# Performance work log

Hardware: AMD Instinct MI355X
Metric: run time of the kernel (lower is better)

## Reference

```python
import jax, jax.numpy as jnp
import numpy as np

N, F = 12288, 512
NEG_INF = jnp.float32(-1e9)  # matches Keras BaseDenseAttention mask additive constant


def setup_inputs() -> dict:
    key = jax.random.key(0)
    k1, k2 = jax.random.split(key)
    features = jax.random.normal(k1, (N, F), dtype=jnp.float32)
    A = jax.random.randint(k2, (N, N), 0, 2).astype(jnp.int32)
    return {"features": features, "A": A}


def reference(features, A):
    # Keras Attention with query=key=value=dropout(features); dropout is identity
    # at inference. use_scale=False -> plain dot-product scores, no 1/sqrt(d).
    scores = jnp.einsum("nf,mf->nm", features, features)          # [N, N]
    scores = jnp.where(A > 0, scores, NEG_INF)                    # mask non-edges
    attn = jax.nn.softmax(scores, axis=-1)                        # softmax over keys
    return jnp.einsum("nm,mf->nf", attn, features)                # [N, F]
```

## Files before the change

kernel.cpp:

```cpp
#include <hip/hip_runtime.h>
#include <cstddef>
#include <cstdint>

#define NN 12288
#define FF 512
#define NWORDS (NN / 32)
#define NKT (NN / 128)

using half8 = __attribute__((ext_vector_type(8))) _Float16;
using half4 = __attribute__((ext_vector_type(4))) _Float16;
using f32x4 = __attribute__((ext_vector_type(4))) float;

constexpr float MASK_NEG = -1e9f;

__device__ __forceinline__ void gll16(const void* g, void* l) {
    __builtin_amdgcn_global_load_lds((const __attribute__((address_space(1))) void*)g,
                                     (__attribute__((address_space(3))) void*)l, 16, 0, 0);
}

#define PHASE(N)                                                        \
    do {                                                                \
        asm volatile("s_waitcnt vmcnt(" #N ")" ::: "memory");           \
        __builtin_amdgcn_s_barrier();                                   \
        __builtin_amdgcn_sched_barrier(0);                              \
    } while (0)

__global__ __launch_bounds__(256)
void compress_mask_kernel(const int* __restrict__ Amat, uint32_t* __restrict__ Abits) {
    const size_t W = (size_t)blockIdx.x * blockDim.x + threadIdx.x;
    const int4* p = reinterpret_cast<const int4*>(Amat + W * 32);
    uint32_t b = 0;
#pragma unroll
    for (int q = 0; q < 8; ++q) {
        const int4 v = p[q];
        b |= (uint32_t)(v.x > 0) << (4 * q + 0);
        b |= (uint32_t)(v.y > 0) << (4 * q + 1);
        b |= (uint32_t)(v.z > 0) << (4 * q + 2);
        b |= (uint32_t)(v.w > 0) << (4 * q + 3);
    }
    Abits[W] = b;
}

__global__ __launch_bounds__(256)
void prep_feat_kernel(const float* __restrict__ in, _Float16* __restrict__ feath,
                      _Float16* __restrict__ featT) {
    __shared__ float tile[32][33];
    const int bi = blockIdx.x;
    const int bj = blockIdx.y;
    const int r  = threadIdx.x >> 3;
    const int c4 = (threadIdx.x & 7) << 2;
    float4 v = *reinterpret_cast<const float4*>(in + (size_t)(bi * 32 + r) * FF + bj * 32 + c4);
    tile[r][c4 + 0] = v.x; tile[r][c4 + 1] = v.y; tile[r][c4 + 2] = v.z; tile[r][c4 + 3] = v.w;
    half4 hr;
    hr[0] = (_Float16)v.x; hr[1] = (_Float16)v.y; hr[2] = (_Float16)v.z; hr[3] = (_Float16)v.w;
    *reinterpret_cast<half4*>(feath + (size_t)(bi * 32 + r) * FF + bj * 32 + c4) = hr;
    __syncthreads();
    half4 h;
#pragma unroll
    for (int k = 0; k < 4; ++k) h[k] = (_Float16)tile[c4 + k][r];
    *reinterpret_cast<half4*>(featT + (size_t)(bj * 32 + r) * NN + bi * 32 + c4) = h;
}

__global__ void cvt_feat_kernel(const float* __restrict__ in, _Float16* __restrict__ out) {
    const size_t i = ((size_t)blockIdx.x * blockDim.x + threadIdx.x) * 8;
    float4 x = *reinterpret_cast<const float4*>(in + i);
    float4 y = *reinterpret_cast<const float4*>(in + i + 4);
    half8 h;
    h[0] = (_Float16)x.x; h[1] = (_Float16)x.y; h[2] = (_Float16)x.z; h[3] = (_Float16)x.w;
    h[4] = (_Float16)y.x; h[5] = (_Float16)y.y; h[6] = (_Float16)y.z; h[7] = (_Float16)y.w;
    *reinterpret_cast<half8*>(out + i) = h;
}

__global__ __launch_bounds__(256)
void gemm1_exp(const _Float16* __restrict__ feath, const uint32_t* __restrict__ Abits,
               _Float16* __restrict__ Pmat, float* __restrict__ m_t, _Float16* __restrict__ s_t) {
    __shared__ alignas(16) _Float16 As[3][128 * 32];
    __shared__ alignas(16) _Float16 Bs[3][128 * 32];
    __shared__ alignas(16) float rowmax2[128][2];
    __shared__ alignas(16) float rowsum2[128][2];

    const int tid = threadIdx.x, lane = tid & 63, wid = tid >> 6;
    const int g = lane >> 4, a = lane & 15;
    const int wr = wid >> 1, wc = wid & 1;
    const int row0 = blockIdx.x * 128, col0 = blockIdx.y * 128;

    f32x4 acc[4][4];
#pragma unroll
    for (int i = 0; i < 4; ++i)
#pragma unroll
        for (int j = 0; j < 4; ++j) acc[i][j] = f32x4{0.f, 0.f, 0.f, 0.f};

    const int lr  = lane >> 2;
    const int sl  = lane & 3;
    const int lsw = (sl ^ ((lr >> 1) & 3)) * 8;
    const int rk  = (a >> 1) & 3;

    auto stage = [&](int buf, int t) {
#pragma unroll
        for (int c = 0; c < 2; ++c) {
            const int ch = wid * 2 + c;
            gll16(feath + (size_t)(row0 + ch * 16 + lr) * FF + t * 32 + lsw, &As[buf][ch * 512]);
            gll16(feath + (size_t)(col0 + ch * 16 + lr) * FF + t * 32 + lsw, &Bs[buf][ch * 512]);
        }
    };

    stage(0, 0);
    stage(1, 1);
#pragma unroll
    for (int t = 0; t < 16; ++t) {
        if (t < 15) PHASE(4);
        else        PHASE(0);
        const int cb = t % 3;
        half8 af[4], bf[4];
#pragma unroll
        for (int rf = 0; rf < 4; ++rf)
            af[rf] = *reinterpret_cast<const half8*>(&As[cb][(64 * wr + 16 * rf + a) * 32 + ((g ^ rk) << 3)]);
#pragma unroll
        for (int cf = 0; cf < 4; ++cf)
            bf[cf] = *reinterpret_cast<const half8*>(&Bs[cb][(64 * wc + 16 * cf + a) * 32 + ((g ^ rk) << 3)]);
#pragma unroll
        for (int rf = 0; rf < 4; ++rf)
#pragma unroll
            for (int cf = 0; cf < 4; ++cf)
                acc[rf][cf] = __builtin_amdgcn_mfma_f32_16x16x32_f16(af[rf], bf[cf], acc[rf][cf], 0, 0, 0);
        if (t + 2 < 16) stage((t + 2) % 3, t + 2);
    }

    const int cw0 = (col0 + 64 * wc) >> 5;
    uint2 am[4][4];
#pragma unroll
    for (int rf = 0; rf < 4; ++rf)
#pragma unroll
        for (int r = 0; r < 4; ++r) {
            const int grow = row0 + 64 * wr + 16 * rf + 4 * g + r;
            am[rf][r] = *reinterpret_cast<const uint2*>(&Abits[(size_t)grow * NWORDS + cw0]);
        }
#pragma unroll
    for (int rf = 0; rf < 4; ++rf)
#pragma unroll
        for (int r = 0; r < 4; ++r)
#pragma unroll
            for (int cf = 0; cf < 4; ++cf) {
                const uint32_t w = (cf < 2) ? am[rf][r].x : am[rf][r].y;
                const uint32_t bit = (w >> (a + 16 * (cf & 1))) & 1u;
                acc[rf][cf][r] = bit ? acc[rf][cf][r] : MASK_NEG;
            }

#pragma unroll
    for (int rf = 0; rf < 4; ++rf)
#pragma unroll
        for (int r = 0; r < 4; ++r) {
            float v = fmaxf(fmaxf(acc[rf][0][r], acc[rf][1][r]), fmaxf(acc[rf][2][r], acc[rf][3][r]));
            v = fmaxf(v, __shfl_xor(v, 1, 16));
            v = fmaxf(v, __shfl_xor(v, 2, 16));
            v = fmaxf(v, __shfl_xor(v, 4, 16));
            v = fmaxf(v, __shfl_xor(v, 8, 16));
            if (a == 0) rowmax2[64 * wr + 16 * rf + 4 * g + r][wc] = v;
        }
    __syncthreads();

#pragma unroll
    for (int rf = 0; rf < 4; ++rf)
#pragma unroll
        for (int r = 0; r < 4; ++r) {
            const int lrow = 64 * wr + 16 * rf + 4 * g + r;
            const float mt = fmaxf(rowmax2[lrow][0], rowmax2[lrow][1]);
            const size_t rbase = (size_t)(row0 + lrow) * NN + col0 + 64 * wc + a;
            float ps = 0.f;
#pragma unroll
            for (int cf = 0; cf < 4; ++cf) {
                const float p = __expf(acc[rf][cf][r] - mt);
                ps += p;
                Pmat[rbase + 16 * cf] = (_Float16)p;
            }
            ps += __shfl_xor(ps, 1, 16);
            ps += __shfl_xor(ps, 2, 16);
            ps += __shfl_xor(ps, 4, 16);
            ps += __shfl_xor(ps, 8, 16);
            if (a == 0) rowsum2[lrow][wc] = ps;
        }
    __syncthreads();
    if (tid < 128) {
        m_t[(size_t)blockIdx.y * NN + row0 + tid] = fmaxf(rowmax2[tid][0], rowmax2[tid][1]);
        s_t[(size_t)blockIdx.y * NN + row0 + tid] = (_Float16)(rowsum2[tid][0] + rowsum2[tid][1]);
    }
}

__global__ __launch_bounds__(256)
void stats_kernel(const float* __restrict__ m_t, const _Float16* __restrict__ s_t,
                  _Float16* __restrict__ sc_t, float* __restrict__ l_row) {
    const int r = blockIdx.x * 256 + threadIdx.x;
    float m = -3.0e38f;
#pragma unroll 4
    for (int kt = 0; kt < NKT; ++kt) m = fmaxf(m, m_t[(size_t)kt * NN + r]);
    float l = 0.f;
#pragma unroll 4
    for (int kt = 0; kt < NKT; ++kt) {
        const float e = __expf(m_t[(size_t)kt * NN + r] - m);
        sc_t[(size_t)kt * NN + r] = (_Float16)e;
        l += e * (float)s_t[(size_t)kt * NN + r];
    }
    l_row[r] = l;
}

__global__ __launch_bounds__(256)
void gemm2_scale(const _Float16* __restrict__ Pmat, const _Float16* __restrict__ featT,
                 const _Float16* __restrict__ sc_t, const float* __restrict__ l_row,
                 float* __restrict__ out) {
    __shared__ alignas(16) _Float16 As[2][128 * 64];
    __shared__ alignas(16) _Float16 Bs[2][64 * 64];

    const int tid = threadIdx.x, lane = tid & 63, wid = tid >> 6;
    const int g = lane >> 4, a = lane & 15;
    const int wr = wid >> 1, wc = wid & 1;
    const int row0 = blockIdx.x * 128, col0 = blockIdx.y * 64;

    f32x4 acc[4][2];
#pragma unroll
    for (int i = 0; i < 4; ++i) { acc[i][0] = f32x4{0.f,0.f,0.f,0.f}; acc[i][1] = f32x4{0.f,0.f,0.f,0.f}; }

    const int l8  = lane >> 3;
    const int sc8 = lane & 7;
    const int xk  = a & 7;
    const size_t scbase = row0 + 64 * wr + a;

    auto stage = [&](int buf, int t) {
#pragma unroll
        for (int c = 0; c < 4; ++c) {
            const int seg = wid * 4 + c;
            const int row = seg * 8 + l8;
            gll16(Pmat + (size_t)(row0 + row) * NN + t * 64 + ((sc8 ^ l8) << 3),
                  &As[buf][seg * 512]);
        }
#pragma unroll
        for (int c = 0; c < 2; ++c) {
            const int seg = wid * 2 + c;
            const int row = seg * 8 + l8;
            gll16(featT + (size_t)(col0 + row) * NN + t * 64 + ((sc8 ^ l8) << 3),
                  &Bs[buf][seg * 512]);
        }
    };

    _Float16 pend[4], sc[4];
#pragma unroll
    for (int rf = 0; rf < 4; ++rf) pend[rf] = sc_t[scbase + 16 * rf];

    stage(0, 0);
    __syncthreads();
    int buf = 0;
    for (int t = 0; t < 192; ++t) {
        if ((t & 1) == 0) {
#pragma unroll
            for (int rf = 0; rf < 4; ++rf) sc[rf] = pend[rf];
            const int ktn = (t >> 1) + 1;
            if (ktn < NKT) {
#pragma unroll
                for (int rf = 0; rf < 4; ++rf)
                    pend[rf] = sc_t[(size_t)ktn * NN + scbase + 16 * rf];
            }
        }
        if (t + 1 < 192) stage(buf ^ 1, t + 1);
#pragma unroll
        for (int kk = 0; kk < 2; ++kk) {
            const int c8r = ((kk << 2) + g) ^ xk;
            half8 af[4], bf[2];
#pragma unroll
            for (int rf = 0; rf < 4; ++rf) {
                const int row = 64 * wr + 16 * rf + a;
                af[rf] = *reinterpret_cast<const half8*>(&As[buf][row * 64 + (c8r << 3)]);
                af[rf] = af[rf] * sc[rf];
            }
#pragma unroll
            for (int cf = 0; cf < 2; ++cf) {
                const int row = 32 * wc + 16 * cf + a;
                bf[cf] = *reinterpret_cast<const half8*>(&Bs[buf][row * 64 + (c8r << 3)]);
            }
#pragma unroll
            for (int rf = 0; rf < 4; ++rf)
#pragma unroll
                for (int cf = 0; cf < 2; ++cf)
                    acc[rf][cf] = __builtin_amdgcn_mfma_f32_16x16x32_f16(af[rf], bf[cf], acc[rf][cf], 0, 0, 0);
        }
        __syncthreads();
        buf ^= 1;
    }

#pragma unroll
    for (int rf = 0; rf < 4; ++rf)
#pragma unroll
        for (int r = 0; r < 4; ++r) {
            const int grow = row0 + 64 * wr + 16 * rf + 4 * g + r;
            const float il = 1.0f / l_row[grow];
#pragma unroll
            for (int cf = 0; cf < 2; ++cf) {
                const int gcol = col0 + 32 * wc + 16 * cf + a;
                out[(size_t)grow * FF + gcol] = acc[rf][cf][r] * il;
            }
        }
}

constexpr int BM_ = 64;
constexpr int BN_ = 64;
constexpr int KV_STRIDE = 520;

template<bool RH>
__global__ __launch_bounds__(512, 2)
void attn_flash(const float* __restrict__ featf, const _Float16* __restrict__ feath,
                const int* __restrict__ Amat, float* __restrict__ out) {
    __shared__ alignas(16) _Float16 kv[BN_ * KV_STRIDE];
    __shared__ alignas(16) _Float16 pbuf[BM_][72];
    __shared__ alignas(16) float pmax[BM_][2];
    __shared__ alignas(16) float psum[BM_][2];
    __shared__ alignas(16) float m_s[BM_];
    __shared__ alignas(16) float l_s[BM_];
    __shared__ alignas(16) float rscale[BM_];

    const int tid  = threadIdx.x;
    const int lane = tid & 63;
    const int wid  = tid >> 6;
    const int g    = lane >> 4;
    const int a    = lane & 15;
    const int rg   = wid >> 1;
    const int ch   = wid & 1;
    const int qrow0 = blockIdx.x * BM_;

    half8 qf[16];
    {
        const int qr = qrow0 + 16 * rg + a;
#pragma unroll
        for (int ks = 0; ks < 16; ++ks) {
            const int f0 = 32 * ks + 8 * g;
            if constexpr (RH) {
                qf[ks] = *reinterpret_cast<const half8*>(feath + (size_t)qr * FF + f0);
            } else {
                const float* sp = featf + (size_t)qr * FF + f0;
                float4 x = *reinterpret_cast<const float4*>(sp);
                float4 y = *reinterpret_cast<const float4*>(sp + 4);
                half8 h;
                h[0] = (_Float16)x.x; h[1] = (_Float16)x.y; h[2] = (_Float16)x.z; h[3] = (_Float16)x.w;
                h[4] = (_Float16)y.x; h[5] = (_Float16)y.y; h[6] = (_Float16)y.z; h[7] = (_Float16)y.w;
                qf[ks] = h;
            }
        }
    }

    f32x4 acc[4][4];
#pragma unroll
    for (int i = 0; i < 4; ++i)
#pragma unroll
        for (int j = 0; j < 4; ++j) acc[i][j] = f32x4{0.f, 0.f, 0.f, 0.f};

    if (tid < BM_) { m_s[tid] = -INFINITY; l_s[tid] = 0.f; }
    __syncthreads();

    for (int kt = 0; kt < NN / BN_; ++kt) {
        const int key0 = kt * BN_;
#pragma unroll
        for (int i = 0; i < 8; ++i) {
            const int flat8 = tid + i * 512;
            const int key   = flat8 >> 6;
            const int b     = flat8 & 63;
            const int slot  = (b + (key >> 3)) & 63;
            _Float16* dst = &kv[key * KV_STRIDE + slot * 8];
            if constexpr (RH) {
                *reinterpret_cast<half8*>(dst) =
                    *reinterpret_cast<const half8*>(feath + (size_t)(key0 + key) * FF + b * 8);
            } else {
                const float* sp = featf + (size_t)(key0 + key) * FF + b * 8;
                float4 x = *reinterpret_cast<const float4*>(sp);
                float4 y = *reinterpret_cast<const float4*>(sp + 4);
                half8 h;
                h[0] = (_Float16)x.x; h[1] = (_Float16)x.y; h[2] = (_Float16)x.z; h[3] = (_Float16)x.w;
                h[4] = (_Float16)y.x; h[5] = (_Float16)y.y; h[6] = (_Float16)y.z; h[7] = (_Float16)y.w;
                *reinterpret_cast<half8*>(dst) = h;
            }
        }

        int am[2][4];
#pragma unroll
        for (int fc = 0; fc < 2; ++fc)
#pragma unroll
            for (int r = 0; r < 4; ++r) {
                const int arow = qrow0 + 16 * rg + 4 * g + r;
                const int acol = key0 + 32 * ch + 16 * fc + a;
                am[fc][r] = Amat[(size_t)arow * NN + acol];
            }
        __syncthreads();

        f32x4 s0{0.f, 0.f, 0.f, 0.f}, s1{0.f, 0.f, 0.f, 0.f};
        const int bk0 = 32 * ch + a;
        const int bk1 = bk0 + 16;
        const int kb0 = bk0 >> 3;
        const int kb1 = bk1 >> 3;
        const _Float16* kr0 = &kv[bk0 * KV_STRIDE];
        const _Float16* kr1 = &kv[bk1 * KV_STRIDE];
#pragma unroll
        for (int ks = 0; ks < 16; ++ks) {
            const int b = 4 * ks + g;
            const half8 bf0 = *reinterpret_cast<const half8*>(kr0 + (((b + kb0) & 63) << 3));
            const half8 bf1 = *reinterpret_cast<const half8*>(kr1 + (((b + kb1) & 63) << 3));
            s0 = __builtin_amdgcn_mfma_f32_16x16x32_f16(qf[ks], bf0, s0, 0, 0, 0);
            s1 = __builtin_amdgcn_mfma_f32_16x16x32_f16(qf[ks], bf1, s1, 0, 0, 0);
        }

        float sv[2][4];
#pragma unroll
        for (int r = 0; r < 4; ++r) {
            sv[0][r] = (am[0][r] > 0) ? s0[r] : MASK_NEG;
            sv[1][r] = (am[1][r] > 0) ? s1[r] : MASK_NEG;
        }
#pragma unroll
        for (int r = 0; r < 4; ++r) {
            float v = fmaxf(sv[0][r], sv[1][r]);
            v = fmaxf(v, __shfl_xor(v, 1, 16));
            v = fmaxf(v, __shfl_xor(v, 2, 16));
            v = fmaxf(v, __shfl_xor(v, 4, 16));
            v = fmaxf(v, __shfl_xor(v, 8, 16));
            if (a == 0) pmax[16 * rg + 4 * g + r][ch] = v;
        }
        __syncthreads();

#pragma unroll
        for (int r = 0; r < 4; ++r) {
            const int row = 16 * rg + 4 * g + r;
            const float mo = m_s[row];
            const float mn = fmaxf(mo, fmaxf(pmax[row][0], pmax[row][1]));
            const float p0 = __expf(sv[0][r] - mn);
            const float p1 = __expf(sv[1][r] - mn);
            pbuf[row][32 * ch + a]      = (_Float16)p0;
            pbuf[row][32 * ch + 16 + a] = (_Float16)p1;
            float ssum = p0 + p1;
            ssum += __shfl_xor(ssum, 1, 16);
            ssum += __shfl_xor(ssum, 2, 16);
            ssum += __shfl_xor(ssum, 4, 16);
            ssum += __shfl_xor(ssum, 8, 16);
            if (a == 0) psum[row][ch] = ssum;
        }
        __syncthreads();

        if (tid < BM_) {
            const float mo = m_s[tid];
            const float mn = fmaxf(mo, fmaxf(pmax[tid][0], pmax[tid][1]));
            const float sc = __expf(mo - mn);
            l_s[tid] = l_s[tid] * sc + psum[tid][0] + psum[tid][1];
            m_s[tid] = mn;
            rscale[tid] = sc;
        }
        __syncthreads();

#pragma unroll
        for (int rf = 0; rf < 4; ++rf) {
            const float4 scv = *reinterpret_cast<const float4*>(&rscale[16 * rf + 4 * g]);
#pragma unroll
            for (int cf = 0; cf < 4; ++cf) {
                acc[rf][cf][0] *= scv.x; acc[rf][cf][1] *= scv.y;
                acc[rf][cf][2] *= scv.z; acc[rf][cf][3] *= scv.w;
            }
        }
#pragma unroll
        for (int kk = 0; kk < 2; ++kk) {
            half8 af[4];
#pragma unroll
            for (int rf = 0; rf < 4; ++rf)
                af[rf] = *reinterpret_cast<const half8*>(&pbuf[16 * rf + a][32 * kk + 8 * g]);
            const int keybase = 32 * kk + 8 * g;
#pragma unroll
            for (int cf = 0; cf < 4; ++cf) {
                const int col  = 64 * wid + 16 * cf + a;
                const int slot = (((col >> 3) + 4 * kk + g) & 63);
                const _Float16* vb = &kv[(size_t)keybase * KV_STRIDE + (slot << 3) + (col & 7)];
                half8 bf;
#pragma unroll
                for (int j = 0; j < 8; ++j)
                    bf[j] = vb[j * KV_STRIDE];
#pragma unroll
                for (int rf = 0; rf < 4; ++rf)
                    acc[rf][cf] = __builtin_amdgcn_mfma_f32_16x16x32_f16(af[rf], bf, acc[rf][cf], 0, 0, 0);
            }
        }
        __syncthreads();
    }

#pragma unroll
    for (int rf = 0; rf < 4; ++rf) {
        const float4 lv = *reinterpret_cast<const float4*>(&l_s[16 * rf + 4 * g]);
        const float inv[4] = {1.f / lv.x, 1.f / lv.y, 1.f / lv.z, 1.f / lv.w};
#pragma unroll
        for (int cf = 0; cf < 4; ++cf) {
            const int col = 64 * wid + 16 * cf + a;
#pragma unroll
            for (int r = 0; r < 4; ++r) {
                out[(size_t)(qrow0 + 16 * rf + 4 * g + r) * FF + col] = acc[rf][cf][r] * inv[r];
            }
        }
    }
}

extern "C" void kernel_launch(void* const* d_in, const int* in_sizes, int n_in,
                              void* d_out, int out_size, void* d_ws, size_t ws_size,
                              hipStream_t stream) {
    const float* features = (const float*)d_in[0];
    const int*   Amat     = (const int*)d_in[1];
    float*       out      = (float*)d_out;

    const size_t P_bytes   = (size_t)NN * NN * 2;
    const size_t f16_bytes = (size_t)NN * FF * 2;
    const size_t sct_bytes = (size_t)NKT * NN * 2;
    const size_t st_bytes  = (size_t)NKT * NN * 2;
    const size_t l_bytes   = (size_t)NN * 4;
    const size_t total     = P_bytes + 2 * f16_bytes + sct_bytes + st_bytes + l_bytes;

    if (ws_size >= total) {
        char* w = (char*)d_ws;
        _Float16* Pmat  = (_Float16*)w;   w += P_bytes;
        _Float16* feath = (_Float16*)w;   w += f16_bytes;
        _Float16* featT = (_Float16*)w;   w += f16_bytes;
        _Float16* sc_t  = (_Float16*)w;   w += sct_bytes;
        _Float16* s_t   = (_Float16*)w;   w += st_bytes;
        float*    l_row = (float*)w;

        uint32_t* Abits = (uint32_t*)d_out;
        float*    m_t   = (float*)((char*)d_out + (size_t)NN * NWORDS * 4);

        compress_mask_kernel<<<(NN * NWORDS) / 256, 256, 0, stream>>>(Amat, Abits);
        prep_feat_kernel<<<dim3(NN / 32, FF / 32), 256, 0, stream>>>(features, feath, featT);
        gemm1_exp<<<dim3(NN / 128, NN / 128), 256, 0, stream>>>(feath, Abits, Pmat, m_t, s_t);
        stats_kernel<<<NN / 256, 256, 0, stream>>>(m_t, s_t, sc_t, l_row);
        gemm2_scale<<<dim3(NN / 128, FF / 64), 256, 0, stream>>>(Pmat, featT, sc_t, l_row, out);
    } else if (ws_size >= f16_bytes) {
        _Float16* feath = (_Float16*)d_ws;
        cvt_feat_kernel<<<(NN * FF) / (256 * 8), 256, 0, stream>>>(features, feath);
        attn_flash<true><<<NN / BM_, 512, 0, stream>>>(features, feath, Amat, out);
    } else {
        attn_flash<false><<<NN / BM_, 512, 0, stream>>>(features, nullptr, Amat, out);
    }
}
```

Baseline: 752.7 us.

## Fuse prepass kernels and triple-buffer gemm2 with waitcnt-based pipelining

The mask compression and feature conversion/transpose kernels are merged into one launch that splits work by block index, saving a kernel launch and letting the two overlap. gemm2_scale changes from a double-buffered 64-wide K tile with XOR swizzle and __syncthreads to a triple-buffered 32-wide K tile, two stages in flight, and vmcnt waits plus raw barriers. This is meant to hide more global-load latency in the second GEMM. The cost is dropping the LDS swizzle, which may bring bank conflicts, and smaller K steps per barrier.

```diff
diff --git a/kernel.cpp b/kernel.cpp
--- a/kernel.cpp
+++ b/kernel.cpp
@@ -6,6 +6,8 @@
 #define FF 512
 #define NWORDS (NN / 32)
 #define NKT (NN / 128)
+#define CMP_BLOCKS ((NN * NWORDS) / 256)
+#define PREP_BLOCKS ((NN / 32) * (FF / 32))
 
 using half8 = __attribute__((ext_vector_type(8))) _Float16;
 using half4 = __attribute__((ext_vector_type(4))) _Float16;
@@ -26,39 +28,41 @@
     } while (0)
 
 __global__ __launch_bounds__(256)
-void compress_mask_kernel(const int* __restrict__ Amat, uint32_t* __restrict__ Abits) {
-    const size_t W = (size_t)blockIdx.x * blockDim.x + threadIdx.x;
-    const int4* p = reinterpret_cast<const int4*>(Amat + W * 32);
-    uint32_t b = 0;
-#pragma unroll
-    for (int q = 0; q < 8; ++q) {
-        const int4 v = p[q];
-        b |= (uint32_t)(v.x > 0) << (4 * q + 0);
-        b |= (uint32_t)(v.y > 0) << (4 * q + 1);
-        b |= (uint32_t)(v.z > 0) << (4 * q + 2);
-        b |= (uint32_t)(v.w > 0) << (4 * q + 3);
-    }
-    Abits[W] = b;
-}
-
-__global__ __launch_bounds__(256)
-void prep_feat_kernel(const float* __restrict__ in, _Float16* __restrict__ feath,
-                      _Float16* __restrict__ featT) {
-    __shared__ float tile[32][33];
-    const int bi = blockIdx.x;
-    const int bj = blockIdx.y;
-    const int r  = threadIdx.x >> 3;
-    const int c4 = (threadIdx.x & 7) << 2;
-    float4 v = *reinterpret_cast<const float4*>(in + (size_t)(bi * 32 + r) * FF + bj * 32 + c4);
-    tile[r][c4 + 0] = v.x; tile[r][c4 + 1] = v.y; tile[r][c4 + 2] = v.z; tile[r][c4 + 3] = v.w;
-    half4 hr;
-    hr[0] = (_Float16)v.x; hr[1] = (_Float16)v.y; hr[2] = (_Float16)v.z; hr[3] = (_Float16)v.w;
-    *reinterpret_cast<half4*>(feath + (size_t)(bi * 32 + r) * FF + bj * 32 + c4) = hr;
-    __syncthreads();
-    half4 h;
-#pragma unroll
-    for (int k = 0; k < 4; ++k) h[k] = (_Float16)tile[c4 + k][r];
-    *reinterpret_cast<half4*>(featT + (size_t)(bj * 32 + r) * NN + bi * 32 + c4) = h;
+void prepass_fused(const int* __restrict__ Amat, uint32_t* __restrict__ Abits,
+                   const float* __restrict__ in, _Float16* __restrict__ feath,
+                   _Float16* __restrict__ featT) {
+    const int bid = blockIdx.x;
+    if (bid < CMP_BLOCKS) {
+        const size_t W = (size_t)bid * 256 + threadIdx.x;
+        const int4* p = reinterpret_cast<const int4*>(Amat + W * 32);
+        uint32_t b = 0;
+#pragma unroll
+        for (int q = 0; q < 8; ++q) {
+            const int4 v = p[q];
+            b |= (uint32_t)(v.x > 0) << (4 * q + 0);
+            b |= (uint32_t)(v.y > 0) << (4 * q + 1);
+            b |= (uint32_t)(v.z > 0) << (4 * q + 2);
+            b |= (uint32_t)(v.w > 0) << (4 * q + 3);
+        }
+        Abits[W] = b;
+    } else {
+        __shared__ float tile[32][33];
+        const int b2 = bid - CMP_BLOCKS;
+        const int bi = b2 % (NN / 32);
+        const int bj = b2 / (NN / 32);
+        const int r  = threadIdx.x >> 3;
+        const int c4 = (threadIdx.x & 7) << 2;
+        float4 v = *reinterpret_cast<const float4*>(in + (size_t)(bi * 32 + r) * FF + bj * 32 + c4);
+        tile[r][c4 + 0] = v.x; tile[r][c4 + 1] = v.y; tile[r][c4 + 2] = v.z; tile[r][c4 + 3] = v.w;
+        half4 hr;
+        hr[0] = (_Float16)v.x; hr[1] = (_Float16)v.y; hr[2] = (_Float16)v.z; hr[3] = (_Float16)v.w;
+        *reinterpret_cast<half4*>(feath + (size_t)(bi * 32 + r) * FF + bj * 32 + c4) = hr;
+        __syncthreads();
+        half4 h;
+#pragma unroll
+        for (int k = 0; k < 4; ++k) h[k] = (_Float16)tile[c4 + k][r];
+        *reinterpret_cast<half4*>(featT + (size_t)(bj * 32 + r) * NN + bi * 32 + c4) = h;
+    }
 }
 
 __global__ void cvt_feat_kernel(const float* __restrict__ in, _Float16* __restrict__ out) {
@@ -207,8 +211,8 @@
 void gemm2_scale(const _Float16* __restrict__ Pmat, const _Float16* __restrict__ featT,
                  const _Float16* __restrict__ sc_t, const float* __restrict__ l_row,
                  float* __restrict__ out) {
-    __shared__ alignas(16) _Float16 As[2][128 * 64];
-    __shared__ alignas(16) _Float16 Bs[2][64 * 64];
+    __shared__ alignas(16) _Float16 As[3][128 * 32];
+    __shared__ alignas(16) _Float16 Bs[3][64 * 32];
 
     const int tid = threadIdx.x, lane = tid & 63, wid = tid >> 6;
     const int g = lane >> 4, a = lane & 15;
@@ -219,26 +223,17 @@
 #pragma unroll
     for (int i = 0; i < 4; ++i) { acc[i][0] = f32x4{0.f,0.f,0.f,0.f}; acc[i][1] = f32x4{0.f,0.f,0.f,0.f}; }
 
-    const int l8  = lane >> 3;
-    const int sc8 = lane & 7;
-    const int xk  = a & 7;
+    const int lr = lane >> 2;
+    const int li = (lane & 3) * 8;
     const size_t scbase = row0 + 64 * wr + a;
 
     auto stage = [&](int buf, int t) {
 #pragma unroll
-        for (int c = 0; c < 4; ++c) {
-            const int seg = wid * 4 + c;
-            const int row = seg * 8 + l8;
-            gll16(Pmat + (size_t)(row0 + row) * NN + t * 64 + ((sc8 ^ l8) << 3),
-                  &As[buf][seg * 512]);
-        }
-#pragma unroll
         for (int c = 0; c < 2; ++c) {
-            const int seg = wid * 2 + c;
-            const int row = seg * 8 + l8;
-            gll16(featT + (size_t)(col0 + row) * NN + t * 64 + ((sc8 ^ l8) << 3),
-                  &Bs[buf][seg * 512]);
-        }
+            const int ch = wid * 2 + c;
+            gll16(Pmat + (size_t)(row0 + ch * 16 + lr) * NN + t * 32 + li, &As[buf][ch * 512]);
+        }
+        gll16(featT + (size_t)(col0 + wid * 16 + lr) * NN + t * 32 + li, &Bs[buf][wid * 512]);
     };
 
     _Float16 pend[4], sc[4];
@@ -246,43 +241,39 @@
     for (int rf = 0; rf < 4; ++rf) pend[rf] = sc_t[scbase + 16 * rf];
 
     stage(0, 0);
-    __syncthreads();
-    int buf = 0;
-    for (int t = 0; t < 192; ++t) {
-        if ((t & 1) == 0) {
-#pragma unroll
-            for (int rf = 0; rf < 4; ++rf) sc[rf] = pend[rf];
-            const int ktn = (t >> 1) + 1;
-            if (ktn < NKT) {
-#pragma unroll
-                for (int rf = 0; rf < 4; ++rf)
-                    pend[rf] = sc_t[(size_t)ktn * NN + scbase + 16 * rf];
-            }
-        }
-        if (t + 1 < 192) stage(buf ^ 1, t + 1);
-#pragma unroll
-        for (int kk = 0; kk < 2; ++kk) {
-            const int c8r = ((kk << 2) + g) ^ xk;
+    stage(1, 1);
+    for (int kt = 0; kt < NKT; ++kt) {
+#pragma unroll
+        for (int tt = 0; tt < 4; ++tt) {
+            const int t = kt * 4 + tt;
+            if (kt == NKT - 1 && tt == 3) PHASE(0);
+            else                          PHASE(3);
+            if (tt == 0) {
+#pragma unroll
+                for (int rf = 0; rf < 4; ++rf) sc[rf] = pend[rf];
+                if (kt + 1 < NKT) {
+#pragma unroll
+                    for (int rf = 0; rf < 4; ++rf)
+                        pend[rf] = sc_t[(size_t)(kt + 1) * NN + scbase + 16 * rf];
+                }
+            }
+            const int cb = t % 3;
             half8 af[4], bf[2];
 #pragma unroll
             for (int rf = 0; rf < 4; ++rf) {
-                const int row = 64 * wr + 16 * rf + a;
-                af[rf] = *reinterpret_cast<const half8*>(&As[buf][row * 64 + (c8r << 3)]);
+                af[rf] = *reinterpret_cast<const half8*>(&As[cb][(64 * wr + 16 * rf + a) * 32 + 8 * g]);
                 af[rf] = af[rf] * sc[rf];
             }
 #pragma unroll
-            for (int cf = 0; cf < 2; ++cf) {
-                const int row = 32 * wc + 16 * cf + a;
-                bf[cf] = *reinterpret_cast<const half8*>(&Bs[buf][row * 64 + (c8r << 3)]);
-            }
+            for (int cf = 0; cf < 2; ++cf)
+                bf[cf] = *reinterpret_cast<const half8*>(&Bs[cb][(32 * wc + 16 * cf + a) * 32 + 8 * g]);
 #pragma unroll
             for (int rf = 0; rf < 4; ++rf)
 #pragma unroll
                 for (int cf = 0; cf < 2; ++cf)
                     acc[rf][cf] = __builtin_amdgcn_mfma_f32_16x16x32_f16(af[rf], bf[cf], acc[rf][cf], 0, 0, 0);
-        }
-        __syncthreads();
-        buf ^= 1;
+            if (t + 2 < 4 * NKT) stage((t + 2) % 3, t + 2);
+        }
     }
 
 #pragma unroll
@@ -522,8 +513,7 @@
         uint32_t* Abits = (uint32_t*)d_out;
         float*    m_t   = (float*)((char*)d_out + (size_t)NN * NWORDS * 4);
 
-        compress_mask_kernel<<<(NN * NWORDS) / 256, 256, 0, stream>>>(Amat, Abits);
-        prep_feat_kernel<<<dim3(NN / 32, FF / 32), 256, 0, stream>>>(features, feath, featT);
+        prepass_fused<<<CMP_BLOCKS + PREP_BLOCKS, 256, 0, stream>>>(Amat, Abits, features, feath, featT);
         gemm1_exp<<<dim3(NN / 128, NN / 128), 256, 0, stream>>>(feath, Abits, Pmat, m_t, s_t);
         stats_kernel<<<NN / 256, 256, 0, stream>>>(m_t, s_t, sc_t, l_row);
         gemm2_scale<<<dim3(NN / 128, FF / 64), 256, 0, stream>>>(Pmat, featT, sc_t, l_row, out);
```

Measured after the change: 773.0 us. 1.03x slower.
